# Optimization experiments

Hardware: AMD Instinct MI355X
Metric: run time of the kernel (lower is better)

The kernel has to match this reference:

```python
import jax, jax.numpy as jnp
import numpy as np

N_EMBD = 256
N_HEAD = 8
BATCH = 4
SEQ = 2048
NEG_BIAS = -1000000000.0


def setup_inputs() -> dict:
    key = jax.random.key(0)
    ks = jax.random.split(key, 5)
    scale = 1.0 / np.sqrt(N_EMBD)
    x = jax.random.normal(ks[0], (BATCH, SEQ, N_EMBD), dtype=jnp.float32)
    # torch Linear weight layout: (out_features, in_features)
    Wq = jax.random.normal(ks[1], (N_EMBD * N_HEAD, N_EMBD), dtype=jnp.float32) * scale
    Wk = jax.random.normal(ks[2], (N_EMBD * N_HEAD, N_EMBD), dtype=jnp.float32) * scale
    Wv = jax.random.normal(ks[3], (N_EMBD * N_HEAD, N_EMBD), dtype=jnp.float32) * scale
    Wo = jax.random.normal(ks[4], (N_EMBD, N_EMBD * N_HEAD), dtype=jnp.float32) * scale / np.sqrt(N_HEAD)
    return {"x": x, "Wq": Wq, "Wk": Wk, "Wv": Wv, "Wo": Wo}


def reference(x, Wq, Wk, Wv, Wo):
    B, L, E = x.shape
    H, D = N_HEAD, N_EMBD  # d_head == n_embd in this module
    # projections: x @ W.T, then split heads -> (B, H, L, D)
    def proj(W):
        y = jnp.einsum('ble,fe->blf', x, W)  # (B, L, H*D)
        return y.reshape(B, L, H, D).transpose(0, 2, 1, 3)
    q, k, v = proj(Wq), proj(Wk), proj(Wv)
    scores = jnp.einsum('bhld,bhmd->bhlm', q, k) * (E ** -0.5)
    # first (non-causal) softmax over full rows
    attn = jax.nn.softmax(scores, axis=-1)
    # causal mask replaces disallowed probs with large negative bias, then softmax again
    causal = jnp.tril(jnp.ones((L, L), dtype=bool))
    attn = jnp.where(causal[None, None], attn, jnp.asarray(NEG_BIAS, attn.dtype))
    attn = jax.nn.softmax(attn, axis=-1)
    out = jnp.einsum('bhlm,bhmd->bhld', attn, v)  # (B, H, L, D)
    out = out.transpose(0, 2, 1, 3).reshape(B, L, H * D)
    return jnp.einsum('blf,ef->ble', out, Wo)  # (B, L, E)
```

## Files before the change

### kernel.cpp

```cpp
#include <hip/hip_runtime.h>
#include <stdint.h>

typedef unsigned short ushort_t;
typedef __attribute__((ext_vector_type(8))) short bf16x8;
typedef __attribute__((ext_vector_type(4))) float f32x4;
typedef __attribute__((ext_vector_type(4))) unsigned short us4;

#define DEV __device__ __forceinline__

DEV ushort_t f2bf(float f) {
    unsigned int u = __float_as_uint(f);
    u += 0x7fffu + ((u >> 16) & 1u);
    return (ushort_t)(u >> 16);
}

DEV void async16(const ushort_t* g, ushort_t* l) {
    __builtin_amdgcn_global_load_lds(
        (const __attribute__((address_space(1))) void*)g,
        (__attribute__((address_space(3))) void*)l,
        16, 0, 0);
}

__global__ void convert_kernel(const float* __restrict__ x, const float* __restrict__ wq,
                               const float* __restrict__ wk, const float* __restrict__ wv,
                               const float* __restrict__ wo,
                               ushort_t* __restrict__ xb, ushort_t* __restrict__ wqb,
                               ushort_t* __restrict__ wkb, ushort_t* __restrict__ wvb,
                               ushort_t* __restrict__ wob)
{
    const int i = blockIdx.x * 256 + threadIdx.x;
    const float* src; ushort_t* dst; int off;
    if (i < 524288)      { src = x;  dst = xb;  off = i; }
    else if (i < 655360) { src = wq; dst = wqb; off = i - 524288; }
    else if (i < 786432) { src = wk; dst = wkb; off = i - 655360; }
    else if (i < 917504) { src = wv; dst = wvb; off = i - 786432; }
    else                 { src = wo; dst = wob; off = i - 917504; }
    const float4 v = ((const float4*)src)[off];
    us4 o;
    o[0] = f2bf(v.x); o[1] = f2bf(v.y); o[2] = f2bf(v.z); o[3] = f2bf(v.w);
    ((us4*)dst)[off] = o;
}

__global__ __launch_bounds__(256, 2) void qkv_gemm_kernel(
    const ushort_t* __restrict__ A, const ushort_t* __restrict__ wq,
    const ushort_t* __restrict__ wk, const ushort_t* __restrict__ wv,
    ushort_t* __restrict__ q_out, ushort_t* __restrict__ k_out,
    ushort_t* __restrict__ vt_out)
{
    __shared__ ushort_t At[128 * 64];
    __shared__ ushort_t Bt[128 * 64];

    const int K = 256, N = 2048;
    const int z = blockIdx.z;
    const ushort_t* Bm = (z == 0) ? wq : (z == 1) ? wk : wv;

    const int tid  = threadIdx.x;
    const int wave = tid >> 6;
    const int lane = tid & 63;
    const int quad = lane >> 4;
    const int l15  = lane & 15;
    const int mhalf = wave >> 1;
    const int nhalf = wave & 1;
    const int m0 = blockIdx.x * 128;
    const int n0 = blockIdx.y * 128;

    f32x4 acc[4][4];
#pragma unroll
    for (int mf = 0; mf < 4; ++mf)
#pragma unroll
        for (int nf = 0; nf < 4; ++nf)
#pragma unroll
            for (int r = 0; r < 4; ++r) acc[mf][nf][r] = 0.f;

    const int crow = (lane & 7) ^ (lane >> 3);

    for (int k0 = 0; k0 < K; k0 += 64) {
        __syncthreads();
#pragma unroll
        for (int t = 0; t < 4; ++t) {
            const int row = wave * 32 + t * 8 + (lane >> 3);
            async16(A + (size_t)(m0 + row) * K + k0 + crow * 8,
                    At + (wave * 32 + t * 8) * 64 + lane * 8);
            async16(Bm + (size_t)(n0 + row) * K + k0 + crow * 8,
                    Bt + (wave * 32 + t * 8) * 64 + lane * 8);
        }
        __syncthreads();
#pragma unroll
        for (int ks = 0; ks < 2; ++ks) {
            bf16x8 af[4], bf[4];
#pragma unroll
            for (int mf = 0; mf < 4; ++mf) {
                const int ml = mhalf * 64 + mf * 16 + l15;
                const int c = (ks * 4 + quad) ^ (ml & 7);
                af[mf] = *(const bf16x8*)(At + ml * 64 + c * 8);
            }
#pragma unroll
            for (int nf = 0; nf < 4; ++nf) {
                const int nl = nhalf * 64 + nf * 16 + l15;
                const int c = (ks * 4 + quad) ^ (nl & 7);
                bf[nf] = *(const bf16x8*)(Bt + nl * 64 + c * 8);
            }
#pragma unroll
            for (int mf = 0; mf < 4; ++mf)
#pragma unroll
                for (int nf = 0; nf < 4; ++nf)
                    acc[mf][nf] = __builtin_amdgcn_mfma_f32_16x16x32_bf16(
                        af[mf], bf[nf], acc[mf][nf], 0, 0, 0);
        }
    }

    if (z == 2) {
#pragma unroll
        for (int mf = 0; mf < 4; ++mf)
#pragma unroll
            for (int nf = 0; nf < 4; ++nf) {
                const int row = m0 + mhalf * 64 + mf * 16 + quad * 4;
                const int col = n0 + nhalf * 64 + nf * 16 + l15;
                const int b_ = row >> 11, l_ = row & 2047;
                const int h_ = col >> 8, d_ = col & 255;
                us4 pk;
#pragma unroll
                for (int r = 0; r < 4; ++r) pk[r] = f2bf(acc[mf][nf][r]);
                *(us4*)(vt_out + (((size_t)(b_ * 8 + h_) * 256 + d_) * 2048 + l_)) = pk;
            }
    } else {
        ushort_t* Cout = z ? k_out : q_out;
#pragma unroll
        for (int mf = 0; mf < 4; ++mf)
#pragma unroll
            for (int nf = 0; nf < 4; ++nf)
#pragma unroll
                for (int r = 0; r < 4; ++r) {
                    const int row = m0 + mhalf * 64 + mf * 16 + quad * 4 + r;
                    const int col = n0 + nhalf * 64 + nf * 16 + l15;
                    Cout[(size_t)row * N + col] = f2bf(acc[mf][nf][r]);
                }
    }
}

__global__ __launch_bounds__(256, 2) void out_gemm_kernel(
    const ushort_t* __restrict__ A, const ushort_t* __restrict__ Bm,
    float* __restrict__ Cout, int M, int N, int K)
{
    __shared__ ushort_t At[128 * 64];
    __shared__ ushort_t Bt[128 * 64];

    const int tid  = threadIdx.x;
    const int wave = tid >> 6;
    const int lane = tid & 63;
    const int quad = lane >> 4;
    const int l15  = lane & 15;
    const int mhalf = wave >> 1;
    const int nhalf = wave & 1;
    const int m0 = blockIdx.x * 128;
    const int n0 = blockIdx.y * 128;

    f32x4 acc[4][4];
#pragma unroll
    for (int mf = 0; mf < 4; ++mf)
#pragma unroll
        for (int nf = 0; nf < 4; ++nf)
#pragma unroll
            for (int r = 0; r < 4; ++r) acc[mf][nf][r] = 0.f;

    const int crow = (lane & 7) ^ (lane >> 3);

    for (int k0 = 0; k0 < K; k0 += 64) {
        __syncthreads();
#pragma unroll
        for (int t = 0; t < 4; ++t) {
            const int row = wave * 32 + t * 8 + (lane >> 3);
            async16(A + (size_t)(m0 + row) * K + k0 + crow * 8,
                    At + (wave * 32 + t * 8) * 64 + lane * 8);
            async16(Bm + (size_t)(n0 + row) * K + k0 + crow * 8,
                    Bt + (wave * 32 + t * 8) * 64 + lane * 8);
        }
        __syncthreads();
#pragma unroll
        for (int ks = 0; ks < 2; ++ks) {
            bf16x8 af[4], bf[4];
#pragma unroll
            for (int mf = 0; mf < 4; ++mf) {
                const int ml = mhalf * 64 + mf * 16 + l15;
                const int c = (ks * 4 + quad) ^ (ml & 7);
                af[mf] = *(const bf16x8*)(At + ml * 64 + c * 8);
            }
#pragma unroll
            for (int nf = 0; nf < 4; ++nf) {
                const int nl = nhalf * 64 + nf * 16 + l15;
                const int c = (ks * 4 + quad) ^ (nl & 7);
                bf[nf] = *(const bf16x8*)(Bt + nl * 64 + c * 8);
            }
#pragma unroll
            for (int mf = 0; mf < 4; ++mf)
#pragma unroll
                for (int nf = 0; nf < 4; ++nf)
                    acc[mf][nf] = __builtin_amdgcn_mfma_f32_16x16x32_bf16(
                        af[mf], bf[nf], acc[mf][nf], 0, 0, 0);
        }
    }

#pragma unroll
    for (int mf = 0; mf < 4; ++mf)
#pragma unroll
        for (int nf = 0; nf < 4; ++nf)
#pragma unroll
            for (int r = 0; r < 4; ++r) {
                const int row = m0 + mhalf * 64 + mf * 16 + quad * 4 + r;
                const int col = n0 + nhalf * 64 + nf * 16 + l15;
                Cout[(size_t)row * N + col] = acc[mf][nf][r];
            }
}

__global__ __launch_bounds__(256, 4) void pass1_kernel(
    const ushort_t* __restrict__ q_ws, const ushort_t* __restrict__ k_ws,
    float* __restrict__ rz_ws)
{
    __shared__ ushort_t Kt[64 * 256];
    __shared__ float zred[2][64];

    const float SCALE = 0.0625f;
    const int tid  = threadIdx.x;
    const int wave = tid >> 6;
    const int lane = tid & 63;
    const int quad = lane >> 4;
    const int l15  = lane & 15;
    const int ihalf = wave >> 1;
    const int jhalf = wave & 1;

    const int g  = blockIdx.x;
    const int bh = ((g >> 8) << 3) | (g & 7);
    const int it = (g >> 3) & 31;
    const int b = bh >> 3, h = bh & 7;
    const int i0 = it * 64;

    const size_t qkbase = (size_t)b * 2048 * 2048 + (size_t)h * 256;

    bf16x8 qf[2][8];
#pragma unroll
    for (int ng = 0; ng < 2; ++ng) {
        const int i_l = ihalf * 32 + ng * 16 + l15;
        const ushort_t* qr = q_ws + qkbase + (size_t)(i0 + i_l) * 2048;
#pragma unroll
        for (int ks = 0; ks < 8; ++ks)
            qf[ng][ks] = *(const bf16x8*)(qr + ks * 32 + quad * 8);
    }

    float z[2] = {0.f, 0.f};

    for (int jt = 0; jt < 32; ++jt) {
        const int j0 = jt * 64;
        __syncthreads();
        {
            const ushort_t* kb = k_ws + qkbase + (size_t)j0 * 2048;
#pragma unroll
            for (int t = 0; t < 8; ++t) {
                const int row = wave * 16 + t * 2 + (lane >> 5);
                const int c = (lane & 31) ^ (row & 7);
                async16(kb + (size_t)row * 2048 + c * 8,
                        Kt + (wave * 16 + t * 2) * 256 + lane * 8);
            }
        }
        __syncthreads();

        f32x4 sacc[2][2];
#pragma unroll
        for (int a = 0; a < 2; ++a)
#pragma unroll
            for (int c = 0; c < 2; ++c)
#pragma unroll
                for (int r = 0; r < 4; ++r) sacc[a][c][r] = 0.f;

#pragma unroll
        for (int ks = 0; ks < 8; ++ks) {
            bf16x8 af[2];
#pragma unroll
            for (int mg = 0; mg < 2; ++mg) {
                const int j_l = jhalf * 32 + mg * 16 + l15;
                const int c = (ks * 4 + quad) ^ (j_l & 7);
                af[mg] = *(const bf16x8*)(Kt + j_l * 256 + c * 8);
            }
#pragma unroll
            for (int mg = 0; mg < 2; ++mg)
#pragma unroll
                for (int ng = 0; ng < 2; ++ng)
                    sacc[mg][ng] = __builtin_amdgcn_mfma_f32_16x16x32_bf16(
                        af[mg], qf[ng][ks], sacc[mg][ng], 0, 0, 0);
        }

#pragma unroll
        for (int ng = 0; ng < 2; ++ng)
#pragma unroll
            for (int mg = 0; mg < 2; ++mg)
#pragma unroll
                for (int r = 0; r < 4; ++r)
                    z[ng] += __expf(sacc[mg][ng][r] * SCALE);
    }

#pragma unroll
    for (int ng = 0; ng < 2; ++ng) {
        z[ng] += __shfl_xor(z[ng], 16);
        z[ng] += __shfl_xor(z[ng], 32);
    }
    __syncthreads();
    if (quad == 0) {
#pragma unroll
        for (int ng = 0; ng < 2; ++ng) {
            const int i_l = ihalf * 32 + ng * 16 + l15;
            zred[jhalf][i_l] = z[ng];
        }
    }
    __syncthreads();
    if (tid < 64)
        rz_ws[(size_t)bh * 2048 + i0 + tid] = 1.0f / (zred[0][tid] + zred[1][tid]);
}

__global__ __launch_bounds__(256, 2) void pass2_kernel(
    const ushort_t* __restrict__ q_ws, const ushort_t* __restrict__ k_ws,
    const ushort_t* __restrict__ vt_ws, const float* __restrict__ rz_ws,
    ushort_t* __restrict__ attn_out)
{
    __shared__ ushort_t smem[36864];
    ushort_t* Kt = smem;
    ushort_t* Vt = smem + 16384;
    ushort_t* Wt = smem + 32768;

    const float SCALE = 0.0625f;
    const int tid  = threadIdx.x;
    const int wave = tid >> 6;
    const int lane = tid & 63;
    const int quad = lane >> 4;
    const int l15  = lane & 15;
    const int ihalf = wave >> 1;
    const int jhalf = wave & 1;

    const int g  = blockIdx.x;
    const int bh = ((g >> 8) << 3) | (g & 7);
    const int it = 31 - ((g >> 3) & 31);
    const int b = bh >> 3, h = bh & 7;
    const int i0 = it * 64;

    const size_t qkbase = (size_t)b * 2048 * 2048 + (size_t)h * 256;

    bf16x8 qf[2][8];
#pragma unroll
    for (int ng = 0; ng < 2; ++ng) {
        const int i_l = ihalf * 32 + ng * 16 + l15;
        const ushort_t* qr = q_ws + qkbase + (size_t)(i0 + i_l) * 2048;
#pragma unroll
        for (int ks = 0; ks < 8; ++ks)
            qf[ng][ks] = *(const bf16x8*)(qr + ks * 32 + quad * 8);
    }

    float rzrow[2];
#pragma unroll
    for (int ng = 0; ng < 2; ++ng) {
        const int i_l = ihalf * 32 + ng * 16 + l15;
        rzrow[ng] = rz_ws[(size_t)bh * 2048 + i0 + i_l];
    }

    f32x4 oacc[2][8];
#pragma unroll
    for (int mg = 0; mg < 2; ++mg)
#pragma unroll
        for (int nf = 0; nf < 8; ++nf)
#pragma unroll
            for (int r = 0; r < 4; ++r) oacc[mg][nf][r] = 0.f;
    float den[2] = {0.f, 0.f};

    for (int jt = 0; jt <= it; ++jt) {
        const int j0 = jt * 64;
        const bool diag = (jt == it);
        __syncthreads();
        {
            const ushort_t* kb = k_ws + qkbase + (size_t)j0 * 2048;
#pragma unroll
            for (int t = 0; t < 8; ++t) {
                const int row = wave * 16 + t * 2 + (lane >> 5);
                const int c = (lane & 31) ^ (row & 7);
                async16(kb + (size_t)row * 2048 + c * 8,
                        Kt + (wave * 16 + t * 2) * 256 + lane * 8);
            }
            const ushort_t* vb = vt_ws + (size_t)bh * 256 * 2048 + j0;
#pragma unroll
            for (int t = 0; t < 8; ++t) {
                const int row = wave * 64 + t * 8 + (lane >> 3);
                const int c = (lane & 7) ^ (row & 7);
                async16(vb + (size_t)row * 2048 + c * 8,
                        Vt + (wave * 64 + t * 8) * 64 + lane * 8);
            }
        }
        __syncthreads();

        f32x4 sacc[2][2];
#pragma unroll
        for (int a = 0; a < 2; ++a)
#pragma unroll
            for (int c = 0; c < 2; ++c)
#pragma unroll
                for (int r = 0; r < 4; ++r) sacc[a][c][r] = 0.f;

#pragma unroll
        for (int ks = 0; ks < 8; ++ks) {
            bf16x8 af[2];
#pragma unroll
            for (int mg = 0; mg < 2; ++mg) {
                const int j_l = jhalf * 32 + mg * 16 + l15;
                const int c = (ks * 4 + quad) ^ (j_l & 7);
                af[mg] = *(const bf16x8*)(Kt + j_l * 256 + c * 8);
            }
#pragma unroll
            for (int mg = 0; mg < 2; ++mg)
#pragma unroll
                for (int ng = 0; ng < 2; ++ng)
                    sacc[mg][ng] = __builtin_amdgcn_mfma_f32_16x16x32_bf16(
                        af[mg], qf[ng][ks], sacc[mg][ng], 0, 0, 0);
        }

#pragma unroll
        for (int mg = 0; mg < 2; ++mg) {
#pragma unroll
            for (int ng = 0; ng < 2; ++ng) {
                const int i_l = ihalf * 32 + ng * 16 + l15;
                const int jb = jhalf * 32 + mg * 16 + quad * 4;
                us4 wp;
#pragma unroll
                for (int r = 0; r < 4; ++r) {
                    const float p = __expf(sacc[mg][ng][r] * SCALE) * rzrow[ng];
                    float w = __expf(p);
                    if (diag && (jb + r > i_l)) w = 0.f;
                    den[ng] += w;
                    wp[r] = f2bf(w);
                }
                const int c = (jb >> 3) ^ (i_l & 7);
                *(us4*)(Wt + i_l * 64 + c * 8 + (jb & 7)) = wp;
            }
        }
        __syncthreads();

#pragma unroll
        for (int ks = 0; ks < 2; ++ks) {
            bf16x8 aw[2];
#pragma unroll
            for (int mg = 0; mg < 2; ++mg) {
                const int i_l = ihalf * 32 + mg * 16 + l15;
                const int c = (ks * 4 + quad) ^ (i_l & 7);
                aw[mg] = *(const bf16x8*)(Wt + i_l * 64 + c * 8);
            }
#pragma unroll
            for (int nf = 0; nf < 8; ++nf) {
                const int d = jhalf * 128 + nf * 16 + l15;
                const int c = (ks * 4 + quad) ^ (d & 7);
                const bf16x8 bv = *(const bf16x8*)(Vt + d * 64 + c * 8);
                oacc[0][nf] = __builtin_amdgcn_mfma_f32_16x16x32_bf16(aw[0], bv, oacc[0][nf], 0, 0, 0);
                oacc[1][nf] = __builtin_amdgcn_mfma_f32_16x16x32_bf16(aw[1], bv, oacc[1][nf], 0, 0, 0);
            }
        }
    }

    __syncthreads();
    {
        float* dbuf = (float*)Kt;
#pragma unroll
        for (int ng = 0; ng < 2; ++ng) {
            const int i_l = ihalf * 32 + ng * 16 + l15;
            dbuf[(jhalf * 4 + quad) * 64 + i_l] = den[ng];
        }
    }
    __syncthreads();
    if (tid < 64) {
        const float* dbuf = (const float*)Kt;
        float s = 0.f;
#pragma unroll
        for (int p = 0; p < 8; ++p) s += dbuf[p * 64 + tid];
        ((float*)Kt)[512 + tid] = 1.0f / s;
    }
    __syncthreads();
    {
        const float* rden = (const float*)Kt + 512;
#pragma unroll
        for (int mg = 0; mg < 2; ++mg) {
#pragma unroll
            for (int r = 0; r < 4; ++r) {
                const int row = ihalf * 32 + mg * 16 + quad * 4 + r;
                const float rd = rden[row];
#pragma unroll
                for (int nf = 0; nf < 8; ++nf) {
                    const int d = jhalf * 128 + nf * 16 + l15;
                    const int xu = (d >> 3) ^ (row & 31);
                    Vt[row * 256 + xu * 8 + (d & 7)] = f2bf(oacc[mg][nf][r] * rd);
                }
            }
        }
    }
    __syncthreads();
    {
        const int row = tid >> 2;
        const int q4  = tid & 3;
        const ushort_t* Vr = Vt + row * 256;
        ushort_t* orow = attn_out + qkbase + (size_t)(i0 + row) * 2048 + q4 * 64;
#pragma unroll
        for (int k = 0; k < 8; ++k) {
            const int xu = (q4 * 8 + k) ^ (row & 31);
            *(bf16x8*)(orow + k * 8) = *(const bf16x8*)(Vr + xu * 8);
        }
    }
}

extern "C" void kernel_launch(void* const* d_in, const int* in_sizes, int n_in,
                              void* d_out, int out_size, void* d_ws, size_t ws_size,
                              hipStream_t stream) {
    const float* x  = (const float*)d_in[0];
    const float* Wq = (const float*)d_in[1];
    const float* Wk = (const float*)d_in[2];
    const float* Wv = (const float*)d_in[3];
    const float* Wo = (const float*)d_in[4];

    char* ws = (char*)d_ws;
    ushort_t* xb    = (ushort_t*)(ws);
    ushort_t* wqb   = (ushort_t*)(ws + 4194304);
    ushort_t* wkb   = (ushort_t*)(ws + 5242880);
    ushort_t* wvb   = (ushort_t*)(ws + 6291456);
    ushort_t* wob   = (ushort_t*)(ws + 7340032);
    ushort_t* q_ws  = (ushort_t*)(ws + 8388608);
    ushort_t* k_ws  = (ushort_t*)(ws + 41943040);
    ushort_t* vt_ws = (ushort_t*)(ws + 75497472);
    ushort_t* ao_ws = (ushort_t*)(ws + 109051904);
    float*    rz_ws = (float*)   (ws + 142606336);

    convert_kernel<<<4096, 256, 0, stream>>>(x, Wq, Wk, Wv, Wo, xb, wqb, wkb, wvb, wob);

    qkv_gemm_kernel<<<dim3(64, 16, 3), 256, 0, stream>>>(
        xb, wqb, wkb, wvb, q_ws, k_ws, vt_ws);

    pass1_kernel<<<1024, 256, 0, stream>>>(q_ws, k_ws, rz_ws);
    pass2_kernel<<<1024, 256, 0, stream>>>(q_ws, k_ws, vt_ws, rz_ws, ao_ws);

    out_gemm_kernel<<<dim3(64, 2), 256, 0, stream>>>(ao_ws, wob, (float*)d_out, 8192, 256, 2048);
}
```

Before: 356.8 us.

## Split-K output GEMM, exp2-based softmax, and direct attention output stores

Adds a split-K version of the output projection GEMM. It uses 4 K-slices across 512 blocks in place of 128, writes fp32 partial tiles to workspace, and sums them in a separate reduction kernel. It only runs when the workspace is large enough. The softmax exponentials are rewritten as exp2 with pre-folded log2e scale factors, and the pass2 epilogue now stores to global memory directly instead of staging through swizzled LDS. The split-K path aims to fill the GPU better for the small output GEMM, at the cost of extra partial-sum traffic and a launch. The direct stores drop a sync and an LDS round trip but give narrower, less coalesced writes.

New measurement: 371.8 us. +4.2%, slower.

```diff
diff --git a/kernel.cpp b/kernel.cpp
--- a/kernel.cpp
+++ b/kernel.cpp
@@ -7,6 +7,9 @@
 typedef __attribute__((ext_vector_type(4))) unsigned short us4;
 
 #define DEV __device__ __forceinline__
+
+#define LOG2E 1.44269504088896f
+#define SCL2  0.09016844006f
 
 DEV ushort_t f2bf(float f) {
     unsigned int u = __float_as_uint(f);
@@ -138,9 +141,9 @@
     }
 }
 
-__global__ __launch_bounds__(256, 2) void out_gemm_kernel(
+__global__ __launch_bounds__(256, 2) void out_gemm_splitk_kernel(
     const ushort_t* __restrict__ A, const ushort_t* __restrict__ Bm,
-    float* __restrict__ Cout, int M, int N, int K)
+    float* __restrict__ Pout, int M, int N, int K)
 {
     __shared__ ushort_t At[128 * 64];
     __shared__ ushort_t Bt[128 * 64];
@@ -154,6 +157,7 @@
     const int nhalf = wave & 1;
     const int m0 = blockIdx.x * 128;
     const int n0 = blockIdx.y * 128;
+    const int ks0 = blockIdx.z * 512;
 
     f32x4 acc[4][4];
 #pragma unroll
@@ -165,7 +169,7 @@
 
     const int crow = (lane & 7) ^ (lane >> 3);
 
-    for (int k0 = 0; k0 < K; k0 += 64) {
+    for (int k0 = ks0; k0 < ks0 + 512; k0 += 64) {
         __syncthreads();
 #pragma unroll
         for (int t = 0; t < 4; ++t) {
@@ -200,6 +204,95 @@
         }
     }
 
+    float* Cp = Pout + (size_t)blockIdx.z * M * N;
+#pragma unroll
+    for (int mf = 0; mf < 4; ++mf)
+#pragma unroll
+        for (int nf = 0; nf < 4; ++nf)
+#pragma unroll
+            for (int r = 0; r < 4; ++r) {
+                const int row = m0 + mhalf * 64 + mf * 16 + quad * 4 + r;
+                const int col = n0 + nhalf * 64 + nf * 16 + l15;
+                Cp[(size_t)row * N + col] = acc[mf][nf][r];
+            }
+}
+
+__global__ void reduce4_kernel(const float4* __restrict__ p, float4* __restrict__ out)
+{
+    const int i = blockIdx.x * 256 + threadIdx.x;
+    float4 a = p[i];
+    const float4 b = p[i + 524288];
+    const float4 c = p[i + 1048576];
+    const float4 d = p[i + 1572864];
+    a.x += b.x + c.x + d.x;
+    a.y += b.y + c.y + d.y;
+    a.z += b.z + c.z + d.z;
+    a.w += b.w + c.w + d.w;
+    out[i] = a;
+}
+
+__global__ __launch_bounds__(256, 2) void out_gemm_kernel(
+    const ushort_t* __restrict__ A, const ushort_t* __restrict__ Bm,
+    float* __restrict__ Cout, int M, int N, int K)
+{
+    __shared__ ushort_t At[128 * 64];
+    __shared__ ushort_t Bt[128 * 64];
+
+    const int tid  = threadIdx.x;
+    const int wave = tid >> 6;
+    const int lane = tid & 63;
+    const int quad = lane >> 4;
+    const int l15  = lane & 15;
+    const int mhalf = wave >> 1;
+    const int nhalf = wave & 1;
+    const int m0 = blockIdx.x * 128;
+    const int n0 = blockIdx.y * 128;
+
+    f32x4 acc[4][4];
+#pragma unroll
+    for (int mf = 0; mf < 4; ++mf)
+#pragma unroll
+        for (int nf = 0; nf < 4; ++nf)
+#pragma unroll
+            for (int r = 0; r < 4; ++r) acc[mf][nf][r] = 0.f;
+
+    const int crow = (lane & 7) ^ (lane >> 3);
+
+    for (int k0 = 0; k0 < K; k0 += 64) {
+        __syncthreads();
+#pragma unroll
+        for (int t = 0; t < 4; ++t) {
+            const int row = wave * 32 + t * 8 + (lane >> 3);
+            async16(A + (size_t)(m0 + row) * K + k0 + crow * 8,
+                    At + (wave * 32 + t * 8) * 64 + lane * 8);
+            async16(Bm + (size_t)(n0 + row) * K + k0 + crow * 8,
+                    Bt + (wave * 32 + t * 8) * 64 + lane * 8);
+        }
+        __syncthreads();
+#pragma unroll
+        for (int ks = 0; ks < 2; ++ks) {
+            bf16x8 af[4], bf[4];
+#pragma unroll
+            for (int mf = 0; mf < 4; ++mf) {
+                const int ml = mhalf * 64 + mf * 16 + l15;
+                const int c = (ks * 4 + quad) ^ (ml & 7);
+                af[mf] = *(const bf16x8*)(At + ml * 64 + c * 8);
+            }
+#pragma unroll
+            for (int nf = 0; nf < 4; ++nf) {
+                const int nl = nhalf * 64 + nf * 16 + l15;
+                const int c = (ks * 4 + quad) ^ (nl & 7);
+                bf[nf] = *(const bf16x8*)(Bt + nl * 64 + c * 8);
+            }
+#pragma unroll
+            for (int mf = 0; mf < 4; ++mf)
+#pragma unroll
+                for (int nf = 0; nf < 4; ++nf)
+                    acc[mf][nf] = __builtin_amdgcn_mfma_f32_16x16x32_bf16(
+                        af[mf], bf[nf], acc[mf][nf], 0, 0, 0);
+        }
+    }
+
 #pragma unroll
     for (int mf = 0; mf < 4; ++mf)
 #pragma unroll
@@ -219,7 +312,6 @@
     __shared__ ushort_t Kt[64 * 256];
     __shared__ float zred[2][64];
 
-    const float SCALE = 0.0625f;
     const int tid  = threadIdx.x;
     const int wave = tid >> 6;
     const int lane = tid & 63;
@@ -294,7 +386,7 @@
             for (int mg = 0; mg < 2; ++mg)
 #pragma unroll
                 for (int r = 0; r < 4; ++r)
-                    z[ng] += __expf(sacc[mg][ng][r] * SCALE);
+                    z[ng] += __builtin_exp2f(sacc[mg][ng][r] * SCL2);
     }
 
 #pragma unroll
@@ -325,7 +417,6 @@
     ushort_t* Vt = smem + 16384;
     ushort_t* Wt = smem + 32768;
 
-    const float SCALE = 0.0625f;
     const int tid  = threadIdx.x;
     const int wave = tid >> 6;
     const int lane = tid & 63;
@@ -426,8 +517,8 @@
                 us4 wp;
 #pragma unroll
                 for (int r = 0; r < 4; ++r) {
-                    const float p = __expf(sacc[mg][ng][r] * SCALE) * rzrow[ng];
-                    float w = __expf(p);
+                    const float p = __builtin_exp2f(sacc[mg][ng][r] * SCL2) * rzrow[ng];
+                    float w = __builtin_exp2f(p * LOG2E);
                     if (diag && (jb + r > i_l)) w = 0.f;
                     den[ng] += w;
                     wp[r] = f2bf(w);
@@ -482,27 +573,15 @@
         for (int mg = 0; mg < 2; ++mg) {
 #pragma unroll
             for (int r = 0; r < 4; ++r) {
-                const int row = ihalf * 32 + mg * 16 + quad * 4 + r;
-                const float rd = rden[row];
+                const int i_l = ihalf * 32 + mg * 16 + quad * 4 + r;
+                const float rd = rden[i_l];
+                ushort_t* orow = attn_out + qkbase + (size_t)(i0 + i_l) * 2048;
 #pragma unroll
                 for (int nf = 0; nf < 8; ++nf) {
                     const int d = jhalf * 128 + nf * 16 + l15;
-                    const int xu = (d >> 3) ^ (row & 31);
-                    Vt[row * 256 + xu * 8 + (d & 7)] = f2bf(oacc[mg][nf][r] * rd);
+                    orow[d] = f2bf(oacc[mg][nf][r] * rd);
                 }
             }
-        }
-    }
-    __syncthreads();
-    {
-        const int row = tid >> 2;
-        const int q4  = tid & 3;
-        const ushort_t* Vr = Vt + row * 256;
-        ushort_t* orow = attn_out + qkbase + (size_t)(i0 + row) * 2048 + q4 * 64;
-#pragma unroll
-        for (int k = 0; k < 8; ++k) {
-            const int xu = (q4 * 8 + k) ^ (row & 31);
-            *(bf16x8*)(orow + k * 8) = *(const bf16x8*)(Vr + xu * 8);
         }
     }
 }
@@ -528,6 +607,11 @@
     ushort_t* ao_ws = (ushort_t*)(ws + 109051904);
     float*    rz_ws = (float*)   (ws + 142606336);
 
+    const size_t PG_OFF = 142868480ull;
+    const size_t PG_END = PG_OFF + 33554432ull;
+    const bool use_splitk = ws_size >= PG_END;
+    float* pg_ws = (float*)(ws + PG_OFF);
+
     convert_kernel<<<4096, 256, 0, stream>>>(x, Wq, Wk, Wv, Wo, xb, wqb, wkb, wvb, wob);
 
     qkv_gemm_kernel<<<dim3(64, 16, 3), 256, 0, stream>>>(
@@ -536,5 +620,13 @@
     pass1_kernel<<<1024, 256, 0, stream>>>(q_ws, k_ws, rz_ws);
     pass2_kernel<<<1024, 256, 0, stream>>>(q_ws, k_ws, vt_ws, rz_ws, ao_ws);
 
-    out_gemm_kernel<<<dim3(64, 2), 256, 0, stream>>>(ao_ws, wob, (float*)d_out, 8192, 256, 2048);
-}
+    if (use_splitk) {
+        out_gemm_splitk_kernel<<<dim3(64, 2, 4), 256, 0, stream>>>(
+            ao_ws, wob, pg_ws, 8192, 256, 2048);
+        reduce4_kernel<<<2048, 256, 0, stream>>>(
+            (const float4*)pg_ws, (float4*)d_out);
+    } else {
+        out_gemm_kernel<<<dim3(64, 2), 256, 0, stream>>>(
+            ao_ws, wob, (float*)d_out, 8192, 256, 2048);
+    }
+}
```
